# Kernel tuning notes

Hardware: AMD Instinct MI355X
Metric: run time of the kernel (lower is better)

Reference implementation:

```python
import jax, jax.numpy as jnp
import numpy as np

NEG_SLOPE = 0.01  # torch F.leaky_relu default


def setup_inputs() -> dict:
    key = jax.random.key(0)
    k1, k2, k3, k4 = jax.random.split(key, 4)
    B, N, F_in, F_out = 16, 2048, 128, 128
    stdv = 1.0 / np.sqrt(F_out)
    h = jax.random.normal(k1, (B, N, F_in), dtype=jnp.float32)
    adj = jax.random.uniform(k2, (B, N, N), dtype=jnp.float32)
    W = jax.random.uniform(k3, (F_in, F_out), minval=-stdv, maxval=stdv, dtype=jnp.float32)
    a = jax.random.uniform(k4, (2 * F_out, 1), minval=-stdv, maxval=stdv, dtype=jnp.float32)
    return {"h": h, "adj": adj, "W": W, "a": a}


def reference(h, adj, W, a):
    # Wh: [B, N, F_out]
    Wh = jnp.matmul(h, W)
    F_out = W.shape[1]
    a1 = a[:F_out, 0]  # [F_out]
    a2 = a[F_out:, 0]  # [F_out]
    # concat-score factorizes: e[b,i,j] = leaky(Wh[b,i]@a1 + Wh[b,j]@a2)
    f1 = jnp.einsum('bnf,f->bn', Wh, a1)  # [B, N]
    f2 = jnp.einsum('bnf,f->bn', Wh, a2)  # [B, N]
    e = jax.nn.leaky_relu(f1[:, :, None] + f2[:, None, :], negative_slope=NEG_SLOPE)  # [B,N,N]
    # NOTE: original softmax is over dim=1 (row index i), faithfully preserved
    attention = jax.nn.softmax(e, axis=1)
    h_prime = jnp.einsum('bij,bjf->bif', attention, Wh)  # bmm
    return h_prime
```

## Files before the change

kernel.cpp:

```cpp
#include <hip/hip_runtime.h>

#define BB 16
#define NN 2048
#define FF 128
#define NEG 0.01f
#define CH 128
#define CL (NN / CH)

__global__ __launch_bounds__(256) void k_wh(const float* __restrict__ h,
                                            const float* __restrict__ Wg,
                                            const float* __restrict__ a,
                                            float* __restrict__ Wh,
                                            float* __restrict__ f1,
                                            float* __restrict__ f2) {
    __shared__ float Ws[64 * 128];
    __shared__ float hsT[64 * 36];

    const int tid  = threadIdx.x;
    const int fg   = tid & 31;
    const int slot = tid >> 5;
    const int f4   = fg * 4;
    const int rowBase = blockIdx.x * 32;

    float acc[4][4];
#pragma unroll
    for (int r = 0; r < 4; ++r)
#pragma unroll
        for (int c = 0; c < 4; ++c) acc[r][c] = 0.f;

    const float4* Wg4 = (const float4*)Wg;
    const float4* hg4 = (const float4*)h;

    for (int kh = 0; kh < 128; kh += 64) {
        __syncthreads();
        for (int idx = tid; idx < 64 * 32; idx += 256) {
            int kk = idx >> 5, ff = idx & 31;
            ((float4*)Ws)[kk * 32 + ff] = Wg4[(size_t)(kh + kk) * 32 + ff];
        }
#pragma unroll
        for (int pass = 0; pass < 2; ++pass) {
            int idx = pass * 256 + tid;
            int kq = idx & 15, row = idx >> 4;
            float4 h4 = hg4[(size_t)(rowBase + row) * 32 + (kh >> 2) + kq];
            hsT[(kq * 4 + 0) * 36 + row] = h4.x;
            hsT[(kq * 4 + 1) * 36 + row] = h4.y;
            hsT[(kq * 4 + 2) * 36 + row] = h4.z;
            hsT[(kq * 4 + 3) * 36 + row] = h4.w;
        }
        __syncthreads();
#pragma unroll 8
        for (int kk = 0; kk < 64; ++kk) {
            float4 wv = *(const float4*)&Ws[kk * 128 + f4];
            float4 hv = *(const float4*)&hsT[kk * 36 + slot * 4];
            acc[0][0] += hv.x * wv.x; acc[0][1] += hv.x * wv.y; acc[0][2] += hv.x * wv.z; acc[0][3] += hv.x * wv.w;
            acc[1][0] += hv.y * wv.x; acc[1][1] += hv.y * wv.y; acc[1][2] += hv.y * wv.z; acc[1][3] += hv.y * wv.w;
            acc[2][0] += hv.z * wv.x; acc[2][1] += hv.z * wv.y; acc[2][2] += hv.z * wv.z; acc[2][3] += hv.z * wv.w;
            acc[3][0] += hv.w * wv.x; acc[3][1] += hv.w * wv.y; acc[3][2] += hv.w * wv.z; acc[3][3] += hv.w * wv.w;
        }
    }

    const float4* ag4 = (const float4*)a;
    float4 a1v = ag4[fg];
    float4 a2v = ag4[32 + fg];

#pragma unroll
    for (int r = 0; r < 4; ++r) {
        int row = rowBase + slot * 4 + r;
        float4 o; o.x = acc[r][0]; o.y = acc[r][1]; o.z = acc[r][2]; o.w = acc[r][3];
        *(float4*)&Wh[(size_t)row * 128 + f4] = o;
        float p1 = acc[r][0] * a1v.x + acc[r][1] * a1v.y + acc[r][2] * a1v.z + acc[r][3] * a1v.w;
        float p2 = acc[r][0] * a2v.x + acc[r][1] * a2v.y + acc[r][2] * a2v.z + acc[r][3] * a2v.w;
#pragma unroll
        for (int m = 16; m >= 1; m >>= 1) {
            p1 += __shfl_xor(p1, m);
            p2 += __shfl_xor(p2, m);
        }
        if (fg == 0) { f1[row] = p1; f2[row] = p2; }
    }
}

__device__ __forceinline__ float wave_incl_scan(float s, int lane) {
#pragma unroll
    for (int m = 1; m <= 32; m <<= 1) {
        float o = __shfl_up(s, m);
        if (lane >= m) s += o;
    }
    return s;
}

template<bool WITHIDX>
__device__ __forceinline__ void cex_shfl(float& v0, float& v1, int& i0, int& i1,
                                         int tid, int j, int k) {
    const int  pj    = j >> 1;
    const bool islow = ((tid & pj) == 0);
    const bool up    = (((tid << 1) & k) == 0);
    float o0 = __shfl_xor(v0, pj);
    float o1 = __shfl_xor(v1, pj);
    int oi0 = 0, oi1 = 0;
    if (WITHIDX) { oi0 = __shfl_xor(i0, pj); oi1 = __shfl_xor(i1, pj); }
    {
        float vl = islow ? v0 : o0, vu = islow ? o0 : v0;
        if ((vl > vu) == up) { v0 = o0; if (WITHIDX) i0 = oi0; }
    }
    {
        float vl = islow ? v1 : o1, vu = islow ? o1 : v1;
        if ((vl > vu) == up) { v1 = o1; if (WITHIDX) i1 = oi1; }
    }
}

template<bool WITHIDX>
__device__ __forceinline__ void cex_intra(float& v0, float& v1, int& i0, int& i1,
                                          int tid, int k) {
    const bool up = (((tid << 1) & k) == 0);
    if ((v0 > v1) == up) {
        float tv = v0; v0 = v1; v1 = tv;
        if (WITHIDX) { int ti = i0; i0 = i1; i1 = ti; }
    }
}

template<bool WITHIDX>
__device__ __forceinline__ void bitonic2048(float* sKey, int* sIdx,
                                            float v0, float v1, int i0, int i1,
                                            int tid) {
#pragma unroll
    for (int k = 2; k <= 128; k <<= 1) {
#pragma unroll
        for (int j = 64; j >= 2; j >>= 1)
            if (j <= (k >> 1)) cex_shfl<WITHIDX>(v0, v1, i0, i1, tid, j, k);
        cex_intra<WITHIDX>(v0, v1, i0, i1, tid, k);
    }
    sKey[2 * tid] = v0; sKey[2 * tid + 1] = v1;
    if (WITHIDX) { sIdx[2 * tid] = i0; sIdx[2 * tid + 1] = i1; }

    for (int k = 256; k <= NN; k <<= 1) {
        for (int j = k >> 1; j >= 128; j >>= 1) {
            __syncthreads();
            int mask = j - 1;
            int i   = ((tid & ~mask) << 1) | (tid & mask);
            int ixj = i | j;
            bool up = ((i & k) == 0);
            float av = sKey[i], bv = sKey[ixj];
            if ((av > bv) == up) {
                sKey[i] = bv; sKey[ixj] = av;
                if (WITHIDX) { int t2 = sIdx[i]; sIdx[i] = sIdx[ixj]; sIdx[ixj] = t2; }
            }
        }
        __syncthreads();
        v0 = sKey[2 * tid]; v1 = sKey[2 * tid + 1];
        if (WITHIDX) { i0 = sIdx[2 * tid]; i1 = sIdx[2 * tid + 1]; }
#pragma unroll
        for (int j = 64; j >= 2; j >>= 1) cex_shfl<WITHIDX>(v0, v1, i0, i1, tid, j, k);
        cex_intra<WITHIDX>(v0, v1, i0, i1, tid, k);
        sKey[2 * tid] = v0; sKey[2 * tid + 1] = v1;
        if (WITHIDX) { sIdx[2 * tid] = i0; sIdx[2 * tid + 1] = i1; }
    }
}

__global__ __launch_bounds__(1024) void k_sort2(const float* __restrict__ f1,
                                                const float* __restrict__ f2,
                                                float* __restrict__ SF1g,
                                                float* __restrict__ PAg,
                                                float* __restrict__ SAg,
                                                float* __restrict__ SKg,
                                                int* __restrict__ PERM,
                                                int* __restrict__ KIDX,
                                                int* __restrict__ ROWS,
                                                int* __restrict__ BOFF) {
    __shared__ float sKey[NN];
    __shared__ int   sIdx[NN];
    __shared__ float wtot[16];
    __shared__ int   hist[CH];
    __shared__ int   hscan[CH + 1];
    __shared__ int   sbuf[CH];

    const int tid  = threadIdx.x;
    const int lane = tid & 63;
    const int w    = tid >> 6;
    const int b    = blockIdx.x & 15;
    const int task = blockIdx.x >> 4;

    const float* f1b = f1 + b * NN;
    const float* f2b = f2 + b * NN;

    if (task == 0) {
        float2 p = ((const float2*)f1b)[tid];
        int i0 = 0, i1 = 0;
        bitonic2048<false>(sKey, sIdx, p.x, p.y, i0, i1, tid);
    } else {
        float2 p = ((const float2*)f2b)[tid];
        bitonic2048<true>(sKey, sIdx, p.x, p.y, 2 * tid, 2 * tid + 1, tid);
    }
    __syncthreads();

    if (task == 0) {
        for (int i = tid; i < NN; i += 1024) SF1g[b * NN + i] = sKey[i];
        const size_t pbase = (size_t)b * (NN + 1);
        {
            float a0 = expf(NEG * sKey[2 * tid]);
            float a1 = expf(NEG * sKey[2 * tid + 1]);
            float s = a0 + a1;
            float v = wave_incl_scan(s, lane);
            if (lane == 63) wtot[w] = v;
            __syncthreads();
            float off = 0.f;
#pragma unroll
            for (int ww = 0; ww < 16; ++ww) off += (ww < w) ? wtot[ww] : 0.f;
            float excl = off + v - s;
            PAg[pbase + 2 * tid]     = excl;
            PAg[pbase + 2 * tid + 1] = excl + a0;
            if (tid == 1023) PAg[pbase + NN] = off + v;
        }
        __syncthreads();
        {
            float y0 = expf(sKey[NN - 1 - 2 * tid]);
            float y1 = expf(sKey[NN - 2 - 2 * tid]);
            float s = y0 + y1;
            float v = wave_incl_scan(s, lane);
            if (lane == 63) wtot[w] = v;
            __syncthreads();
            float off = 0.f;
#pragma unroll
            for (int ww = 0; ww < 16; ++ww) off += (ww < w) ? wtot[ww] : 0.f;
            SAg[pbase + NN - 1 - 2 * tid] = off + (v - s) + y0;
            SAg[pbase + NN - 2 - 2 * tid] = off + v;
            if (tid == 0) SAg[pbase + NN] = 0.f;
        }
    } else {
        for (int i = tid; i < NN; i += 1024) {
            SKg[b * NN + i]  = sKey[i];
            PERM[b * NN + i] = sIdx[i];
        }
        if (tid < CH) hist[tid] = 0;
        __syncthreads();
        for (int i = tid; i < NN; i += 1024) {
            float tau = -f1b[i];
            int lo = 0, hi = NN;
            while (lo < hi) { int m = (lo + hi) >> 1; if (sKey[m] <= tau) lo = m + 1; else hi = m; }
            KIDX[b * NN + i] = lo;
            int c = lo / CL;
            if (c > CH - 1) c = CH - 1;
            sIdx[i] = c;
            atomicAdd(&hist[c], 1);
        }
        __syncthreads();
        if (tid < CH) sbuf[tid] = hist[tid];
        for (int off = 1; off < CH; off <<= 1) {
            __syncthreads();
            int v = 0;
            if (tid < CH) { v = sbuf[tid]; if (tid >= off) v += sbuf[tid - off]; }
            __syncthreads();
            if (tid < CH) sbuf[tid] = v;
        }
        __syncthreads();
        if (tid == 0) hscan[0] = 0;
        if (tid < CH) hscan[tid + 1] = sbuf[tid];
        __syncthreads();
        if (tid <= CH) BOFF[b * (CH + 1) + tid] = hscan[tid];
        if (tid < CH) hist[tid] = hscan[tid];
        __syncthreads();
        for (int i = tid; i < NN; i += 1024) {
            int c = sIdx[i];
            int pos = atomicAdd(&hist[c], 1);
            ROWS[b * NN + pos] = i;
        }
    }
}

__global__ __launch_bounds__(256) void k_uw(const float* __restrict__ SF1g,
                                            const float* __restrict__ PAg,
                                            const float* __restrict__ SAg,
                                            const float* __restrict__ SKg,
                                            float* __restrict__ Uarr,
                                            float* __restrict__ Warr) {
    __shared__ float sS[NN];
    const int b = blockIdx.x >> 3;
    const int q = blockIdx.x & 7;
    const int tid = threadIdx.x;
    const size_t pbase = (size_t)b * (NN + 1);
    for (int i = tid; i < NN; i += 256) sS[i] = SF1g[b * NN + i];
    __syncthreads();
    const int t = q * 256 + tid;
    float f2v = SKg[b * NN + t];
    float tau = -f2v;
    int lo = 0, hi = NN;
    while (lo < hi) { int m = (lo + hi) >> 1; if (sS[m] <= tau) lo = m + 1; else hi = m; }
    float eS = expf(NEG * f2v);
    float eF = expf(f2v);
    float inv = 1.0f / (eS * PAg[pbase + lo] + eF * SAg[pbase + lo]);
    Uarr[b * NN + t] = eF * inv;
    Warr[b * NN + t] = eS * inv;
}

__global__ __launch_bounds__(128) void k_chunk(const float* __restrict__ Wh,
                                               const float* __restrict__ Uarr,
                                               const float* __restrict__ Warr,
                                               const int* __restrict__ PERM,
                                               float* __restrict__ CU,
                                               float* __restrict__ CW) {
    int blk = blockIdx.x;
    int b = blk / CH, c = blk % CH;
    int f = threadIdx.x;
    int base = b * NN + c * CL;
    const float* Whb = Wh + (size_t)b * NN * FF;
    float aU = 0.f, aW = 0.f;
#pragma unroll
    for (int t = 0; t < CL; ++t) {
        int j = PERM[base + t];
        float uv = Uarr[base + t], wv = Warr[base + t];
        float whv = Whb[(size_t)j * FF + f];
        aU += uv * whv; aW += wv * whv;
    }
    CU[(size_t)blk * FF + f] = aU;
    CW[(size_t)blk * FF + f] = aW;
}

__global__ __launch_bounds__(1024) void k_offsets(float* __restrict__ CU,
                                                  float* __restrict__ CW,
                                                  float* __restrict__ TOT) {
    __shared__ float psU[8][FF];
    __shared__ float psW[8][FF];
    const int b   = blockIdx.x;
    const int f   = threadIdx.x & 127;
    const int seg = threadIdx.x >> 7;
    const size_t base = (size_t)(b * CH + seg * 16) * FF + f;

    float rU[16], rW[16];
    float sU = 0.f, sW = 0.f;
#pragma unroll
    for (int cc = 0; cc < 16; ++cc) {
        rU[cc] = CU[base + (size_t)cc * FF];
        rW[cc] = CW[base + (size_t)cc * FF];
        sU += rU[cc]; sW += rW[cc];
    }
    psU[seg][f] = sU; psW[seg][f] = sW;
    __syncthreads();

    float oU = 0.f, oW = 0.f, tU = 0.f;
#pragma unroll
    for (int s = 0; s < 8; ++s) {
        float pu = psU[s][f], pw = psW[s][f];
        if (s < seg) { oU += pu; oW += pw; }
        tU += pu;
    }
    if (seg == 0) TOT[b * FF + f] = tU;

#pragma unroll
    for (int cc = 0; cc < 16; ++cc) {
        size_t idx = base + (size_t)cc * FF;
        CU[idx] = oU; CW[idx] = oW;
        oU += rU[cc]; oW += rW[cc];
    }
}

__global__ __launch_bounds__(128) void k_emit(const float* __restrict__ Wh,
                                              const float* __restrict__ Uarr,
                                              const float* __restrict__ Warr,
                                              const int* __restrict__ PERM,
                                              const float* __restrict__ CU,
                                              const float* __restrict__ CW,
                                              const float* __restrict__ TOT,
                                              const float* __restrict__ f1,
                                              const int* __restrict__ KIDX,
                                              const int* __restrict__ ROWS,
                                              const int* __restrict__ BOFF,
                                              float* __restrict__ out) {
    __shared__ float pU[CL + 1][FF];
    __shared__ float pW[CL + 1][FF];

    const int blk = blockIdx.x;
    const int b = blk / CH, c = blk % CH;
    const int f = threadIdx.x;

    const int rb = BOFF[b * (CH + 1) + c];
    const int re = BOFF[b * (CH + 1) + c + 1];
    if (rb == re) return;

    float aU = CU[(size_t)blk * FF + f];
    float aW = CW[(size_t)blk * FF + f];
    const float totU = TOT[b * FF + f];

    const int base = b * NN + c * CL;
    const float* Whb = Wh + (size_t)b * NN * FF;
#pragma unroll
    for (int t = 0; t < CL; ++t) {
        pU[t][f] = aU; pW[t][f] = aW;
        int j = PERM[base + t];
        float whv = Whb[(size_t)j * FF + f];
        aU += Uarr[base + t] * whv;
        aW += Warr[base + t] * whv;
    }
    pU[CL][f] = aU; pW[CL][f] = aW;
    __syncthreads();

    for (int idx = rb; idx < re; ++idx) {
        int i = ROWS[b * NN + idx];
        int k = KIDX[b * NN + i];
        int r = k - c * CL;
        float f1v = f1[b * NN + i];
        float alpha = expf(NEG * f1v);
        float beta  = expf(f1v);
        out[((size_t)(b * NN + i)) * FF + f] = alpha * pW[r][f] + beta * (totU - pU[r][f]);
    }
}

extern "C" void kernel_launch(void* const* d_in, const int* in_sizes, int n_in,
                              void* d_out, int out_size, void* d_ws, size_t ws_size,
                              hipStream_t stream) {
    const float* h  = (const float*)d_in[0];
    const float* W  = (const float*)d_in[2];
    const float* a  = (const float*)d_in[3];
    float* out = (float*)d_out;

    float* ws = (float*)d_ws;
    float* Wh   = ws;  ws += (size_t)BB * NN * FF;
    float* f1   = ws;  ws += BB * NN;
    float* f2   = ws;  ws += BB * NN;
    float* SF1  = ws;  ws += BB * NN;
    float* PA   = ws;  ws += BB * (NN + 1);
    float* SA   = ws;  ws += BB * (NN + 1);
    float* SK   = ws;  ws += BB * NN;
    float* Uarr = ws;  ws += BB * NN;
    float* Warr = ws;  ws += BB * NN;
    float* CU   = ws;  ws += (size_t)BB * CH * FF;
    float* CW   = ws;  ws += (size_t)BB * CH * FF;
    float* TOT  = ws;  ws += BB * FF;
    int* PERM = (int*)ws;  ws += BB * NN;
    int* KIDX = (int*)ws;  ws += BB * NN;
    int* ROWS = (int*)ws;  ws += BB * NN;
    int* BOFF = (int*)ws;

    k_wh     <<<(BB * NN) / 32, 256, 0, stream>>>(h, W, a, Wh, f1, f2);
    k_sort2  <<<2 * BB, 1024, 0, stream>>>(f1, f2, SF1, PA, SA, SK, PERM, KIDX, ROWS, BOFF);
    k_uw     <<<BB * 8, 256, 0, stream>>>(SF1, PA, SA, SK, Uarr, Warr);
    k_chunk  <<<BB * CH, 128, 0, stream>>>(Wh, Uarr, Warr, PERM, CU, CW);
    k_offsets<<<BB, 1024, 0, stream>>>(CU, CW, TOT);
    k_emit   <<<BB * CH, 128, 0, stream>>>(Wh, Uarr, Warr, PERM, CU, CW, TOT, f1, KIDX, ROWS, BOFF, out);
}
```

Measured before the change: 373.2 us.

## Compute Wh projection with split-bf16 MFMA instead of FP32 FMA

Rewrites the h@W projection kernel to use 16x16x32 bf16 MFMA instructions, splitting each fp32 value into hi and lo bf16 parts and summing three products to keep near-fp32 accuracy. W is converted into swizzled hi/lo bf16 planes in shared memory, and each wave computes 16 rows by 128 columns. Blocks now cover 64 rows. The aim is to move the GEMM from scalar FMA onto the matrix cores. In exchange, every block redoes the W conversion, Wh stores become scattered scalar writes, and results carry a small precision loss.

```diff
diff --git a/kernel.cpp b/kernel.cpp
--- a/kernel.cpp
+++ b/kernel.cpp
@@ -7,75 +7,114 @@
 #define CH 128
 #define CL (NN / CH)
 
+typedef __attribute__((ext_vector_type(8))) short short8;
+typedef __attribute__((ext_vector_type(4))) float f32x4;
+
+__device__ __forceinline__ unsigned short f2bf_rne(float x) {
+    unsigned int u = __float_as_uint(x);
+    unsigned int r = u + 0x7FFFu + ((u >> 16) & 1u);
+    return (unsigned short)(r >> 16);
+}
+__device__ __forceinline__ float bf2f(unsigned short b) {
+    return __uint_as_float(((unsigned int)b) << 16);
+}
+
 __global__ __launch_bounds__(256) void k_wh(const float* __restrict__ h,
                                             const float* __restrict__ Wg,
                                             const float* __restrict__ a,
                                             float* __restrict__ Wh,
                                             float* __restrict__ f1,
                                             float* __restrict__ f2) {
-    __shared__ float Ws[64 * 128];
-    __shared__ float hsT[64 * 36];
-
-    const int tid  = threadIdx.x;
-    const int fg   = tid & 31;
-    const int slot = tid >> 5;
-    const int f4   = fg * 4;
-    const int rowBase = blockIdx.x * 32;
-
-    float acc[4][4];
-#pragma unroll
-    for (int r = 0; r < 4; ++r)
-#pragma unroll
-        for (int c = 0; c < 4; ++c) acc[r][c] = 0.f;
-
-    const float4* Wg4 = (const float4*)Wg;
-    const float4* hg4 = (const float4*)h;
-
-    for (int kh = 0; kh < 128; kh += 64) {
-        __syncthreads();
-        for (int idx = tid; idx < 64 * 32; idx += 256) {
-            int kk = idx >> 5, ff = idx & 31;
-            ((float4*)Ws)[kk * 32 + ff] = Wg4[(size_t)(kh + kk) * 32 + ff];
-        }
-#pragma unroll
-        for (int pass = 0; pass < 2; ++pass) {
-            int idx = pass * 256 + tid;
-            int kq = idx & 15, row = idx >> 4;
-            float4 h4 = hg4[(size_t)(rowBase + row) * 32 + (kh >> 2) + kq];
-            hsT[(kq * 4 + 0) * 36 + row] = h4.x;
-            hsT[(kq * 4 + 1) * 36 + row] = h4.y;
-            hsT[(kq * 4 + 2) * 36 + row] = h4.z;
-            hsT[(kq * 4 + 3) * 36 + row] = h4.w;
-        }
-        __syncthreads();
-#pragma unroll 8
-        for (int kk = 0; kk < 64; ++kk) {
-            float4 wv = *(const float4*)&Ws[kk * 128 + f4];
-            float4 hv = *(const float4*)&hsT[kk * 36 + slot * 4];
-            acc[0][0] += hv.x * wv.x; acc[0][1] += hv.x * wv.y; acc[0][2] += hv.x * wv.z; acc[0][3] += hv.x * wv.w;
-            acc[1][0] += hv.y * wv.x; acc[1][1] += hv.y * wv.y; acc[1][2] += hv.y * wv.z; acc[1][3] += hv.y * wv.w;
-            acc[2][0] += hv.z * wv.x; acc[2][1] += hv.z * wv.y; acc[2][2] += hv.z * wv.z; acc[2][3] += hv.z * wv.w;
-            acc[3][0] += hv.w * wv.x; acc[3][1] += hv.w * wv.y; acc[3][2] += hv.w * wv.z; acc[3][3] += hv.w * wv.w;
-        }
-    }
-
-    const float4* ag4 = (const float4*)a;
-    float4 a1v = ag4[fg];
-    float4 a2v = ag4[32 + fg];
-
-#pragma unroll
-    for (int r = 0; r < 4; ++r) {
-        int row = rowBase + slot * 4 + r;
-        float4 o; o.x = acc[r][0]; o.y = acc[r][1]; o.z = acc[r][2]; o.w = acc[r][3];
-        *(float4*)&Wh[(size_t)row * 128 + f4] = o;
-        float p1 = acc[r][0] * a1v.x + acc[r][1] * a1v.y + acc[r][2] * a1v.z + acc[r][3] * a1v.w;
-        float p2 = acc[r][0] * a2v.x + acc[r][1] * a2v.y + acc[r][2] * a2v.z + acc[r][3] * a2v.w;
-#pragma unroll
-        for (int m = 16; m >= 1; m >>= 1) {
-            p1 += __shfl_xor(p1, m);
-            p2 += __shfl_xor(p2, m);
-        }
-        if (fg == 0) { f1[row] = p1; f2[row] = p2; }
+    __shared__ __align__(16) unsigned short WTs[2 * 128 * 128];
+
+    const int t = threadIdx.x;
+
+    {
+        const int isLo = t >> 7;
+        const int f    = t & 127;
+        char* plane = (char*)WTs + isLo * 32768;
+#pragma unroll
+        for (int j = 0; j < 16; ++j) {
+            short8 pk;
+#pragma unroll
+            for (int e = 0; e < 8; ++e) {
+                int k = j * 8 + e;
+                float x = Wg[k * 128 + f];
+                unsigned short hb = f2bf_rne(x);
+                if (isLo) hb = f2bf_rne(x - bf2f(hb));
+                pk[e] = (short)hb;
+            }
+            unsigned int byte = f * 256 + (((unsigned)j << 4) ^ ((unsigned)(f & 7) << 4));
+            *(short8*)(plane + byte) = pk;
+        }
+    }
+    __syncthreads();
+
+    const int lane = t & 63;
+    const int wid  = t >> 6;
+    const int r    = lane & 15;
+    const int g    = lane >> 4;
+    const int rowBase = blockIdx.x * 64 + wid * 16;
+    const float* hrow = h + (size_t)(rowBase + r) * 128;
+
+    f32x4 acc[8];
+#pragma unroll
+    for (int nt = 0; nt < 8; ++nt) acc[nt] = (f32x4){0.f, 0.f, 0.f, 0.f};
+
+#pragma unroll
+    for (int ks = 0; ks < 4; ++ks) {
+        float4 v0 = *(const float4*)(hrow + ks * 32 + g * 8);
+        float4 v1 = *(const float4*)(hrow + ks * 32 + g * 8 + 4);
+        float xs[8] = {v0.x, v0.y, v0.z, v0.w, v1.x, v1.y, v1.z, v1.w};
+        short8 Ahi, Alo;
+#pragma unroll
+        for (int e = 0; e < 8; ++e) {
+            unsigned short hb = f2bf_rne(xs[e]);
+            Ahi[e] = (short)hb;
+            Alo[e] = (short)f2bf_rne(xs[e] - bf2f(hb));
+        }
+#pragma unroll
+        for (int nt = 0; nt < 8; ++nt) {
+            int fcol = nt * 16 + r;
+            unsigned int byte = fcol * 256 +
+                ((((unsigned)(ks * 4 + g)) << 4) ^ ((unsigned)(fcol & 7) << 4));
+            short8 Bhi = *(const short8*)((const char*)WTs + byte);
+            short8 Blo = *(const short8*)((const char*)WTs + 32768 + byte);
+            acc[nt] = __builtin_amdgcn_mfma_f32_16x16x32_bf16(Ahi, Bhi, acc[nt], 0, 0, 0);
+            acc[nt] = __builtin_amdgcn_mfma_f32_16x16x32_bf16(Ahi, Blo, acc[nt], 0, 0, 0);
+            acc[nt] = __builtin_amdgcn_mfma_f32_16x16x32_bf16(Alo, Bhi, acc[nt], 0, 0, 0);
+        }
+    }
+
+    float pr1[4] = {0.f, 0.f, 0.f, 0.f};
+    float pr2[4] = {0.f, 0.f, 0.f, 0.f};
+#pragma unroll
+    for (int nt = 0; nt < 8; ++nt) {
+        int col = nt * 16 + r;
+        float av1 = a[col];
+        float av2 = a[128 + col];
+#pragma unroll
+        for (int j = 0; j < 4; ++j) {
+            float v = acc[nt][j];
+            Wh[(size_t)(rowBase + g * 4 + j) * 128 + col] = v;
+            pr1[j] += v * av1;
+            pr2[j] += v * av2;
+        }
+    }
+#pragma unroll
+    for (int j = 0; j < 4; ++j) {
+#pragma unroll
+        for (int m = 1; m < 16; m <<= 1) {
+            pr1[j] += __shfl_xor(pr1[j], m);
+            pr2[j] += __shfl_xor(pr2[j], m);
+        }
+    }
+    if (r == 0) {
+#pragma unroll
+        for (int j = 0; j < 4; ++j) {
+            f1[rowBase + g * 4 + j] = pr1[j];
+            f2[rowBase + g * 4 + j] = pr2[j];
+        }
     }
 }
 
@@ -429,7 +468,7 @@
     int* ROWS = (int*)ws;  ws += BB * NN;
     int* BOFF = (int*)ws;
 
-    k_wh     <<<(BB * NN) / 32, 256, 0, stream>>>(h, W, a, Wh, f1, f2);
+    k_wh     <<<(BB * NN) / 64, 256, 0, stream>>>(h, W, a, Wh, f1, f2);
     k_sort2  <<<2 * BB, 1024, 0, stream>>>(f1, f2, SF1, PA, SA, SK, PERM, KIDX, ROWS, BOFF);
     k_uw     <<<BB * 8, 256, 0, stream>>>(SF1, PA, SA, SK, Uarr, Warr);
     k_chunk  <<<BB * CH, 128, 0, stream>>>(Wh, Uarr, Warr, PERM, CU, CW);
```

Result: slower. 408.2 us (+9.4%).
